# Optimization experiments

Hardware: AMD Instinct MI355X
Metric: run time of the kernel (lower is better)

## Reference

```python
import jax, jax.numpy as jnp
import numpy as np
from jax import lax

B_, H_, W_ = 2, 32, 32
D_MODEL, D_STATE, D_CONV, DT_RANK, K = 192, 16, 3, 12, 4
D_INNER = 2 * D_MODEL


def setup_inputs() -> dict:
    key = jax.random.key(0)
    ks = jax.random.split(key, 10)
    x = jax.random.normal(ks[0], (B_, H_, W_, D_MODEL), jnp.float32)
    x_cross = jax.random.normal(ks[1], (B_, H_, W_, D_MODEL), jnp.float32)
    in_proj_w = jax.random.normal(ks[2], (2 * D_INNER, D_MODEL), jnp.float32) * 0.02
    in_proj_cross_w = jax.random.normal(ks[3], (D_INNER, D_MODEL), jnp.float32) * 0.02
    conv_w = jax.random.normal(ks[4], (D_INNER, 1, D_CONV, D_CONV), jnp.float32) * 0.1  # depthwise
    conv_b = jnp.zeros((D_INNER,), jnp.float32)
    x_proj_weight = jax.random.normal(ks[5], (K, DT_RANK + 2 * D_STATE, D_INNER), jnp.float32) * 0.02
    dt_std = DT_RANK ** -0.5
    dt_projs_weight = jax.random.uniform(ks[6], (K, D_INNER, DT_RANK), jnp.float32, -dt_std, dt_std)
    # inverse-softplus init of dt bias, as in CSS2D.dt_init
    dt = jnp.exp(jax.random.uniform(ks[7], (K, D_INNER), jnp.float32)
                 * (np.log(0.1) - np.log(0.001)) + np.log(0.001))
    dt = jnp.clip(dt, 1e-4, None)
    dt_projs_bias = dt + jnp.log(-jnp.expm1(-dt))
    A_logs = jnp.log(jnp.tile(jnp.arange(1, D_STATE + 1, dtype=jnp.float32)[None, :], (K * D_INNER, 1)))
    Ds = jnp.ones((K * D_INNER,), jnp.float32)
    out_norm_g = jnp.ones((D_INNER,), jnp.float32)
    out_norm_b = jnp.zeros((D_INNER,), jnp.float32)
    out_proj_w = jax.random.normal(ks[8], (D_MODEL, D_INNER), jnp.float32) * 0.02
    return dict(x=x, x_cross=x_cross, in_proj_w=in_proj_w, in_proj_cross_w=in_proj_cross_w,
                conv_w=conv_w, conv_b=conv_b, x_proj_weight=x_proj_weight,
                dt_projs_weight=dt_projs_weight, dt_projs_bias=dt_projs_bias,
                A_logs=A_logs, Ds=Ds, out_norm_g=out_norm_g, out_norm_b=out_norm_b,
                out_proj_w=out_proj_w)


def _css2d_forward(x, x_cross, in_proj_w, in_proj_cross_w, conv_w, conv_b,
                   x_proj_weight, dt_projs_weight, dt_projs_bias, A_logs, Ds,
                   out_norm_g, out_norm_b, out_proj_w):
    B, H, W, _ = x.shape
    L = H * W
    Din, N, R = D_INNER, D_STATE, DT_RANK

    # in projections
    xz = x @ in_proj_w.T                       # [B,H,W,2*Din]
    xp, z = jnp.split(xz, 2, axis=-1)
    xc = x_cross @ in_proj_cross_w.T           # [B,H,W,Din]

    # depthwise conv + SiLU on main branch (NCHW)
    xh = jnp.transpose(xp, (0, 3, 1, 2))
    pad = (D_CONV - 1) // 2
    xh = lax.conv_general_dilated(xh, conv_w, (1, 1), [(pad, pad), (pad, pad)],
                                  dimension_numbers=('NCHW', 'OIHW', 'NCHW'),
                                  feature_group_count=Din)
    xh = jax.nn.silu(xh + conv_b[None, :, None, None])
    xc = jnp.transpose(xc, (0, 3, 1, 2))       # [B,Din,H,W]

    def cross_scan(t):  # [B,Din,H,W] -> [B,4,Din,L]
        a = t.reshape(B, Din, L)
        b = jnp.transpose(t, (0, 1, 3, 2)).reshape(B, Din, L)
        s = jnp.stack([a, b], axis=1)
        return jnp.concatenate([s, jnp.flip(s, axis=-1)], axis=1)

    xs = cross_scan(xh)
    xsc = cross_scan(xc)

    # dt/B/C projections from the cross stream
    x_dbl = jnp.einsum('bkdl,kcd->bkcl', xsc, x_proj_weight)
    dts, Bmat, Cmat = jnp.split(x_dbl, [R, R + N], axis=2)  # [B,K,R,L],[B,K,N,L],[B,K,N,L]
    dts = jnp.einsum('bkrl,kdr->bkdl', dts, dt_projs_weight)

    A = -jnp.exp(A_logs).reshape(K, Din, N)
    delta = jax.nn.softplus(dts + dt_projs_bias[None, :, :, None])  # [B,K,Din,L]

    # selective scan: h_{t} = exp(delta*A)*h_{t-1} + delta*B_t*u_t ; y_t = C_t . h_t
    dA = jnp.exp(jnp.einsum('bkdl,kdn->lbkdn', delta, A))   # [L,B,K,Din,N]
    dBu = jnp.einsum('bkdl,bknl->lbkdn', delta * xs, Bmat)  # [L,B,K,Din,N]
    Ct = jnp.transpose(Cmat, (3, 0, 1, 2))                  # [L,B,K,N]

    def step(h, inp):
        dA_t, dBu_t, c = inp
        h = dA_t * h + dBu_t
        return h, jnp.einsum('bkdn,bkn->bkd', h, c)

    h0 = jnp.zeros((B, K, Din, N), x.dtype)
    _, ys = lax.scan(step, h0, (dA, dBu, Ct))               # ys: [L,B,K,Din]
    out_y = jnp.transpose(ys, (1, 2, 3, 0)) + xs * Ds.reshape(1, K, Din, 1)  # [B,K,Din,L]

    # merge the 4 directions
    inv_y = jnp.flip(out_y[:, 2:4], axis=-1)
    wh = lambda t: jnp.transpose(t.reshape(B, Din, W, H), (0, 1, 3, 2)).reshape(B, Din, L)
    y = out_y[:, 0] + inv_y[:, 0] + wh(out_y[:, 1]) + wh(inv_y[:, 1])
    y = jnp.transpose(y, (0, 2, 1)).reshape(B, H, W, Din)

    # LayerNorm(out_norm)
    mu = jnp.mean(y, axis=-1, keepdims=True)
    var = jnp.mean((y - mu) ** 2, axis=-1, keepdims=True)
    y = (y - mu) * lax.rsqrt(var + 1e-5) * out_norm_g + out_norm_b

    y = y * jax.nn.silu(z)
    return y @ out_proj_w.T


def reference(x, x_cross, in_proj_w, in_proj_cross_w, conv_w, conv_b, x_proj_weight,
              dt_projs_weight, dt_projs_bias, A_logs, Ds, out_norm_g, out_norm_b, out_proj_w):
    return _css2d_forward(x, x_cross, in_proj_w, in_proj_cross_w, conv_w, conv_b,
                          x_proj_weight, dt_projs_weight, dt_projs_bias, A_logs, Ds,
                          out_norm_g, out_norm_b, out_proj_w)
```

## Files before the change

### kernel.cpp

```cpp
#include <hip/hip_runtime.h>
#include <hip/hip_bf16.h>
#include <math.h>

#define BB 2
#define HH 32
#define WW 32
#define LL 1024
#define DM 192
#define DI 384
#define NS 16
#define RR 12
#define KK 4
#define CC 44
#define NC 64
#define LC 16
#define NCH 3072
#define GB 49152
#define XT 8

__device__ __forceinline__ int bfflag(const void* dsv){
  return ((const unsigned*)dsv)[0] != 0x3F800000u;
}
__device__ __forceinline__ float ldin(const void* p, int i, int bf) {
  if (bf) {
    unsigned v = ((const unsigned short*)p)[i];
    return __uint_as_float(v << 16);
  }
  return ((const float*)p)[i];
}
__device__ __forceinline__ float4 ldin4(const void* p, int i, int bf) {
  if (bf) {
    ushort4 u = ((const ushort4*)p)[i >> 2];
    float4 r;
    r.x = __uint_as_float((unsigned)u.x << 16);
    r.y = __uint_as_float((unsigned)u.y << 16);
    r.z = __uint_as_float((unsigned)u.z << 16);
    r.w = __uint_as_float((unsigned)u.w << 16);
    return r;
  }
  return ((const float4*)p)[i >> 2];
}
__device__ __forceinline__ float sigm(float x){ return 1.f/(1.f + __expf(-x)); }
__device__ __forceinline__ float softplusf(float x){ return (x > 20.f) ? x : log1pf(__expf(x)); }

__device__ __forceinline__ int permk(int k, int l){
  if (k == 0) return l;
  if (k == 2) return LL-1-l;
  int lr = (k == 3) ? (LL-1-l) : l;
  return (lr & 31)*WW + (lr >> 5);
}

__global__ __launch_bounds__(192) void k_inproj(const void* x, const void* xcr,
    const void* wi, const void* wc, const void* dsv,
    float* __restrict__ xp, float* __restrict__ z, float* __restrict__ xc){
  const int bf = bfflag(dsv);
  __shared__ float xs_[16][DM];
  const int t = threadIdx.x;
  const int rg = blockIdx.x / 128;
  const int pos0 = (blockIdx.x % 128) * 16;
  const void* src = (rg >= 4) ? xcr : x;
  for (int i = t*4; i < 16*DM; i += 192*4) {
    *(float4*)&(((float*)xs_)[i]) = ldin4(src, pos0*DM + i, bf);
  }
  __syncthreads();
  const int grow = rg*192 + t;
  const void* wb = (grow < 768) ? wi : wc;
  const int wrow = (grow < 768) ? grow : grow - 768;
  float* dst; int o;
  if (grow < 384)      { dst = xp; o = grow; }
  else if (grow < 768) { dst = z;  o = grow - 384; }
  else                 { dst = xc; o = grow - 768; }
  float acc[16];
  #pragma unroll
  for (int p=0;p<16;p++) acc[p]=0.f;
  for (int j=0;j<DM;j+=4) {
    const float4 w4 = ldin4(wb, wrow*DM + j, bf);
    #pragma unroll
    for (int p=0;p<16;p++){
      const float4 xv = *(const float4*)&xs_[p][j];
      acc[p] = fmaf(w4.x, xv.x, acc[p]);
      acc[p] = fmaf(w4.y, xv.y, acc[p]);
      acc[p] = fmaf(w4.z, xv.z, acc[p]);
      acc[p] = fmaf(w4.w, xv.w, acc[p]);
    }
  }
  #pragma unroll
  for (int p=0;p<16;p++) dst[(pos0+p)*DI + o] = acc[p];
}

__global__ __launch_bounds__(256) void k_conv(const float* __restrict__ xp,
    const void* cw, const void* cb, const void* dsv, float* __restrict__ xh){
  const int bf = bfflag(dsv);
  const int idx = blockIdx.x*256 + threadIdx.x;
  const int d = idx % DI;
  const int l = (idx / DI) % LL;
  const int b = idx / (DI*LL);
  const int h = l >> 5, w = l & 31;
  float acc = ldin(cb, d, bf);
  #pragma unroll
  for (int kh=0; kh<3; kh++){
    const int hh = h + kh - 1;
    if (hh < 0 || hh >= HH) continue;
    #pragma unroll
    for (int kw=0; kw<3; kw++){
      const int ww2 = w + kw - 1;
      if (ww2 < 0 || ww2 >= WW) continue;
      acc = fmaf(xp[(b*LL + hh*WW + ww2)*DI + d], ldin(cw, d*9 + kh*3 + kw, bf), acc);
    }
  }
  xh[idx] = acc * sigm(acc);
}

__global__ __launch_bounds__(384) void k_xproj(const float* __restrict__ xc, const void* xpw,
    const void* dtw, const void* dtb, const void* dsv,
    float* __restrict__ delta, float* __restrict__ Bm, float* __restrict__ Cm){
  const int bf = bfflag(dsv);
  const int blk = blockIdx.x;
  const int b = blk >> 9;
  const int k = (blk >> 7) & 3;
  const int l0 = (blk & 127) * XT;
  const int t = threadIdx.x;
  __shared__ float xrow[XT][DI+4];
  __shared__ float dtsS[XT][RR];
  for (int idx = t; idx < XT*96; idx += 384){
    const int j = idx / 96, c = idx % 96;
    const int pl = permk(k, l0 + j);
    *(float4*)&xrow[j][c*4] = *(const float4*)&xc[(b*LL + pl)*DI + c*4];
  }
  __syncthreads();
  if (t < CC*XT){
    const int ch = t >> 3, j = t & 7;
    const int wbase = (k*CC + ch)*DI;
    float a0=0.f, a1=0.f, a2=0.f, a3=0.f;
    for (int c = 0; c < 96; c += 4){
      const float4 w0 = ldin4(xpw, wbase + (c+0)*4, bf);
      const float4 w1 = ldin4(xpw, wbase + (c+1)*4, bf);
      const float4 w2 = ldin4(xpw, wbase + (c+2)*4, bf);
      const float4 w3 = ldin4(xpw, wbase + (c+3)*4, bf);
      const float4 x0 = *(const float4*)&xrow[j][(c+0)*4];
      const float4 x1 = *(const float4*)&xrow[j][(c+1)*4];
      const float4 x2 = *(const float4*)&xrow[j][(c+2)*4];
      const float4 x3 = *(const float4*)&xrow[j][(c+3)*4];
      a0 = fmaf(w0.x,x0.x, fmaf(w0.y,x0.y, fmaf(w0.z,x0.z, fmaf(w0.w,x0.w, a0))));
      a1 = fmaf(w1.x,x1.x, fmaf(w1.y,x1.y, fmaf(w1.z,x1.z, fmaf(w1.w,x1.w, a1))));
      a2 = fmaf(w2.x,x2.x, fmaf(w2.y,x2.y, fmaf(w2.z,x2.z, fmaf(w2.w,x2.w, a2))));
      a3 = fmaf(w3.x,x3.x, fmaf(w3.y,x3.y, fmaf(w3.z,x3.z, fmaf(w3.w,x3.w, a3))));
    }
    const float acc = (a0+a1)+(a2+a3);
    if (ch < RR)           dtsS[j][ch] = acc;
    else if (ch < RR+NS)   Bm[((b*KK+k)*LL + l0+j)*NS + (ch-RR)]    = acc;
    else                   Cm[((b*KK+k)*LL + l0+j)*NS + (ch-RR-NS)] = acc;
  }
  __syncthreads();
  {
    const int d = t;
    float w[RR];
    #pragma unroll
    for (int q = 0; q < 3; q++){
      const float4 w4 = ldin4(dtw, (k*DI+d)*RR + q*4, bf);
      w[q*4+0]=w4.x; w[q*4+1]=w4.y; w[q*4+2]=w4.z; w[q*4+3]=w4.w;
    }
    const float bias = ldin(dtb, k*DI + d, bf);
    #pragma unroll
    for (int j = 0; j < XT; j++){
      float acc = bias;
      #pragma unroll
      for (int r = 0; r < RR; r++) acc = fmaf(w[r], dtsS[j][r], acc);
      xrow[j][d] = softplusf(acc);
    }
  }
  __syncthreads();
  for (int idx = t; idx < XT*96; idx += 384){
    const int j = idx / 96, c = idx % 96;
    *(float4*)&delta[((b*KK+k)*LL + l0+j)*DI + c*4] = *(const float4*)&xrow[j][c*4];
  }
}

__global__ __launch_bounds__(256) void k_scanA(const float* __restrict__ delta,
    const float* __restrict__ xh, const float* __restrict__ Bm,
    const void* alogs, const void* dsv,
    float* __restrict__ Acum, float* __restrict__ Hend){
  const int bf = bfflag(dsv);
  const int c = blockIdx.x / 12;
  const int chain = (blockIdx.x % 12)*256 + threadIdx.x;
  const int d = chain % DI;
  const int k = (chain / DI) & 3;
  const int b = chain / (DI*KK);
  float An[NS];
  #pragma unroll
  for (int q = 0; q < 4; q++){
    const float4 a4 = ldin4(alogs, (k*DI + d)*NS + q*4, bf);
    An[q*4+0] = -__expf(a4.x); An[q*4+1] = -__expf(a4.y);
    An[q*4+2] = -__expf(a4.z); An[q*4+3] = -__expf(a4.w);
  }
  float h[NS], Ac[NS];
  #pragma unroll
  for (int n = 0; n < NS; n++){ h[n] = 0.f; Ac[n] = 1.f; }
  const int lb = (b*KK+k)*LL;
  const int xbase = b*LL*DI + d;
  const int l0 = c*LC;
  #pragma unroll 4
  for (int l = l0; l < l0+LC; l++){
    const float dl = delta[(lb + l)*DI + d];
    const float u  = xh[xbase + permk(k,l)*DI];
    const float dlu = dl*u;
    const float4 B0 = *(const float4*)&Bm[(lb+l)*NS + 0];
    const float4 B1 = *(const float4*)&Bm[(lb+l)*NS + 4];
    const float4 B2 = *(const float4*)&Bm[(lb+l)*NS + 8];
    const float4 B3 = *(const float4*)&Bm[(lb+l)*NS + 12];
    const float Bv[NS] = {B0.x,B0.y,B0.z,B0.w, B1.x,B1.y,B1.z,B1.w,
                          B2.x,B2.y,B2.z,B2.w, B3.x,B3.y,B3.z,B3.w};
    #pragma unroll
    for (int n = 0; n < NS; n++){
      const float e = __expf(dl*An[n]);
      Ac[n] *= e;
      h[n] = fmaf(e, h[n], dlu*Bv[n]);
    }
  }
  const int obase = (c*NCH + chain)*NS;
  #pragma unroll
  for (int q = 0; q < 4; q++){
    *(float4*)&Acum[obase + q*4] = make_float4(Ac[q*4],Ac[q*4+1],Ac[q*4+2],Ac[q*4+3]);
    *(float4*)&Hend[obase + q*4] = make_float4(h[q*4],h[q*4+1],h[q*4+2],h[q*4+3]);
  }
}

__global__ __launch_bounds__(256) void k_scanB(const float* __restrict__ Acum,
    float* __restrict__ Hend){
  const int g = blockIdx.x*256 + threadIdx.x;
  float h = 0.f;
  #pragma unroll 8
  for (int c = 0; c < NC; c++){
    const float a = Acum[c*GB + g];
    const float e = Hend[c*GB + g];
    Hend[c*GB + g] = h;
    h = fmaf(a, h, e);
  }
}

__global__ __launch_bounds__(256) void k_scanC(const float* __restrict__ delta,
    const float* __restrict__ xh, const float* __restrict__ Bm,
    const float* __restrict__ Cm, const void* alogs, const void* dsv,
    const float* __restrict__ Hin, float* __restrict__ ybuf){
  const int bf = bfflag(dsv);
  const int c = blockIdx.x / 12;
  const int chain = (blockIdx.x % 12)*256 + threadIdx.x;
  const int d = chain % DI;
  const int k = (chain / DI) & 3;
  const int b = chain / (DI*KK);
  float An[NS];
  #pragma unroll
  for (int q = 0; q < 4; q++){
    const float4 a4 = ldin4(alogs, (k*DI + d)*NS + q*4, bf);
    An[q*4+0] = -__expf(a4.x); An[q*4+1] = -__expf(a4.y);
    An[q*4+2] = -__expf(a4.z); An[q*4+3] = -__expf(a4.w);
  }
  float h[NS];
  const int ibase = (c*NCH + chain)*NS;
  #pragma unroll
  for (int q = 0; q < 4; q++){
    const float4 h4 = *(const float4*)&Hin[ibase + q*4];
    h[q*4+0]=h4.x; h[q*4+1]=h4.y; h[q*4+2]=h4.z; h[q*4+3]=h4.w;
  }
  const int lb = (b*KK+k)*LL;
  const int xbase = b*LL*DI + d;
  const int l0 = c*LC;
  #pragma unroll 4
  for (int l = l0; l < l0+LC; l++){
    const float dl = delta[(lb + l)*DI + d];
    const float u  = xh[xbase + permk(k,l)*DI];
    const float dlu = dl*u;
    const float4 B0 = *(const float4*)&Bm[(lb+l)*NS + 0];
    const float4 B1 = *(const float4*)&Bm[(lb+l)*NS + 4];
    const float4 B2 = *(const float4*)&Bm[(lb+l)*NS + 8];
    const float4 B3 = *(const float4*)&Bm[(lb+l)*NS + 12];
    const float4 C0 = *(const float4*)&Cm[(lb+l)*NS + 0];
    const float4 C1 = *(const float4*)&Cm[(lb+l)*NS + 4];
    const float4 C2 = *(const float4*)&Cm[(lb+l)*NS + 8];
    const float4 C3 = *(const float4*)&Cm[(lb+l)*NS + 12];
    const float Bv[NS] = {B0.x,B0.y,B0.z,B0.w, B1.x,B1.y,B1.z,B1.w,
                          B2.x,B2.y,B2.z,B2.w, B3.x,B3.y,B3.z,B3.w};
    const float Cv[NS] = {C0.x,C0.y,C0.z,C0.w, C1.x,C1.y,C1.z,C1.w,
                          C2.x,C2.y,C2.z,C2.w, C3.x,C3.y,C3.z,C3.w};
    float y = 0.f;
    #pragma unroll
    for (int n = 0; n < NS; n++){
      const float e = __expf(dl*An[n]);
      h[n] = fmaf(e, h[n], dlu*Bv[n]);
      y = fmaf(h[n], Cv[n], y);
    }
    ybuf[(lb + l)*DI + d] = y;
  }
}

__global__ __launch_bounds__(256) void k_merge(const float* __restrict__ scanY,
    const float* __restrict__ xh, const float* __restrict__ z,
    const void* dsP, const void* gP, const void* bP, const void* woP,
    void* out){
  const int bf = bfflag(dsP);
  const int blk = blockIdx.x;
  const int t = threadIdx.x;
  const int wv = t >> 6, lane = t & 63;
  __shared__ float ygs[8][DI];
  #pragma unroll
  for (int rep = 0; rep < 2; rep++){
    const int j = wv*2 + rep;
    const int pos = blk*8 + j;
    const int b = pos >> 10, l = pos & 1023;
    const int lt = (l & 31)*32 + (l >> 5);
    float yv[6];
    float s = 0.f, s2 = 0.f;
    #pragma unroll
    for (int i = 0; i < 6; i++){
      const int d = i*64 + lane;
      float y = scanY[((b*KK+0)*LL + l        )*DI + d]
              + scanY[((b*KK+2)*LL + (LL-1-l ))*DI + d]
              + scanY[((b*KK+1)*LL + lt       )*DI + d]
              + scanY[((b*KK+3)*LL + (LL-1-lt))*DI + d];
      const float dsum = ldin(dsP, d, bf) + ldin(dsP, DI+d, bf)
                       + ldin(dsP, 2*DI+d, bf) + ldin(dsP, 3*DI+d, bf);
      y = fmaf(xh[(b*LL+l)*DI + d], dsum, y);
      yv[i] = y;
      s += y; s2 = fmaf(y, y, s2);
    }
    #pragma unroll
    for (int m = 1; m < 64; m <<= 1){
      s  += __shfl_xor(s,  m);
      s2 += __shfl_xor(s2, m);
    }
    const float mu = s * (1.f/DI);
    const float var = fmaxf(s2 * (1.f/DI) - mu*mu, 0.f);
    const float rs = rsqrtf(var + 1e-5f);
    #pragma unroll
    for (int i = 0; i < 6; i++){
      const int d = i*64 + lane;
      const float yn = (yv[i]-mu)*rs*ldin(gP, d, bf) + ldin(bP, d, bf);
      const float zg = z[(b*LL+l)*DI + d];
      ygs[j][d] = yn * zg * sigm(zg);
    }
  }
  __syncthreads();
  if (t < DM){
    const int o = t;
    float acc[8];
    #pragma unroll
    for (int j=0;j<8;j++) acc[j] = 0.f;
    for (int c = 0; c < 96; c++){
      const float4 w4 = ldin4(woP, o*DI + c*4, bf);
      #pragma unroll
      for (int j=0;j<8;j++){
        const float4 y4 = *(const float4*)&ygs[j][c*4];
        acc[j] = fmaf(w4.x, y4.x, acc[j]);
        acc[j] = fmaf(w4.y, y4.y, acc[j]);
        acc[j] = fmaf(w4.z, y4.z, acc[j]);
        acc[j] = fmaf(w4.w, y4.w, acc[j]);
      }
    }
    #pragma unroll
    for (int j=0;j<8;j++){
      const int pos = blk*8 + j;
      if (bf) ((__hip_bfloat16*)out)[pos*DM + o] = __float2bfloat16(acc[j]);
      else    ((float*)out)[pos*DM + o] = acc[j];
    }
  }
}

extern "C" void kernel_launch(void* const* d_in, const int* in_sizes, int n_in,
                              void* d_out, int out_size, void* d_ws, size_t ws_size,
                              hipStream_t stream){
  const void* x    = d_in[0];
  const void* xcr  = d_in[1];
  const void* wi   = d_in[2];
  const void* wc   = d_in[3];
  const void* cw   = d_in[4];
  const void* cb   = d_in[5];
  const void* xpw  = d_in[6];
  const void* dtw  = d_in[7];
  const void* dtb  = d_in[8];
  const void* alog = d_in[9];
  const void* dsv  = d_in[10];
  const void* gno  = d_in[11];
  const void* bno  = d_in[12];
  const void* wo   = d_in[13];

  float* ws = (float*)d_ws;
  float* xp    = ws + 16;
  float* z     = xp    + (size_t)BB*LL*DI;
  float* xc    = z     + (size_t)BB*LL*DI;
  float* xh    = xc    + (size_t)BB*LL*DI;
  float* delta = xh    + (size_t)BB*LL*DI;
  float* Bm    = delta + (size_t)BB*KK*LL*DI;
  float* Cm    = Bm    + (size_t)BB*KK*LL*NS;
  float* Acum  = Cm    + (size_t)BB*KK*LL*NS;
  float* Hend  = Acum  + (size_t)GB*NC;
  float* ybuf  = Hend  + (size_t)GB*NC;

  k_inproj<<<6*128, 192, 0, stream>>>(x, xcr, wi, wc, dsv, xp, z, xc);
  k_conv  <<<BB*LL*DI/256, 256, 0, stream>>>(xp, cw, cb, dsv, xh);
  k_xproj <<<BB*KK*(LL/XT), 384, 0, stream>>>(xc, xpw, dtw, dtb, dsv, delta, Bm, Cm);
  k_scanA <<<NCH*NC/256, 256, 0, stream>>>(delta, xh, Bm, alog, dsv, Acum, Hend);
  k_scanB <<<GB/256, 256, 0, stream>>>(Acum, Hend);
  k_scanC <<<NCH*NC/256, 256, 0, stream>>>(delta, xh, Bm, Cm, alog, dsv, Hend, ybuf);
  k_merge <<<BB*LL/8, 256, 0, stream>>>(ybuf, xh, z, dsv, gno, bno, wo, d_out);
}
```

Baseline: 242.9 us.

## Tile in-projection GEMM with 64x64 shared-memory blocks and 4x4 register tiles

Rewrites the input projection kernel as a classic shared-memory tiled GEMM. Each block stages 64 positions and 64 weight rows per 64-wide K chunk and computes a 4x4 output tile per thread, writing results with float4 stores. Previously every thread streamed its own weight row from global memory with no reuse and wrote scattered scalars. The new version adds transposed shared-memory stores (padded to 65) that can cause bank conflicts, and the float4 reads from the padded rows may be misaligned.

```diff
diff --git a/kernel.cpp b/kernel.cpp
--- a/kernel.cpp
+++ b/kernel.cpp
@@ -50,42 +50,61 @@
   return (lr & 31)*WW + (lr >> 5);
 }
 
-__global__ __launch_bounds__(192) void k_inproj(const void* x, const void* xcr,
+__global__ __launch_bounds__(256) void k_inproj(const void* x, const void* xcr,
     const void* wi, const void* wc, const void* dsv,
-    float* __restrict__ xp, float* __restrict__ z, float* __restrict__ xc){
+    float* __restrict__ xp, float* __restrict__ z, float* __restrict__ xcd){
   const int bf = bfflag(dsv);
-  __shared__ float xs_[16][DM];
+  __shared__ float As[64][65];
+  __shared__ float Ws[64][65];
+  const int mb = blockIdx.x & 31;
+  const int nb = blockIdx.x >> 5;
+  const int pos0 = mb*64;
+  const int row0g = nb*64;
+  const void* src  = (row0g < 768) ? x  : xcr;
+  const void* wsrc = (row0g < 768) ? wi : wc;
+  const int wrow0 = (row0g < 768) ? row0g : row0g - 768;
   const int t = threadIdx.x;
-  const int rg = blockIdx.x / 128;
-  const int pos0 = (blockIdx.x % 128) * 16;
-  const void* src = (rg >= 4) ? xcr : x;
-  for (int i = t*4; i < 16*DM; i += 192*4) {
-    *(float4*)&(((float*)xs_)[i]) = ldin4(src, pos0*DM + i, bf);
-  }
-  __syncthreads();
-  const int grow = rg*192 + t;
-  const void* wb = (grow < 768) ? wi : wc;
-  const int wrow = (grow < 768) ? grow : grow - 768;
-  float* dst; int o;
-  if (grow < 384)      { dst = xp; o = grow; }
-  else if (grow < 768) { dst = z;  o = grow - 384; }
-  else                 { dst = xc; o = grow - 768; }
-  float acc[16];
-  #pragma unroll
-  for (int p=0;p<16;p++) acc[p]=0.f;
-  for (int j=0;j<DM;j+=4) {
-    const float4 w4 = ldin4(wb, wrow*DM + j, bf);
-    #pragma unroll
-    for (int p=0;p<16;p++){
-      const float4 xv = *(const float4*)&xs_[p][j];
-      acc[p] = fmaf(w4.x, xv.x, acc[p]);
-      acc[p] = fmaf(w4.y, xv.y, acc[p]);
-      acc[p] = fmaf(w4.z, xv.z, acc[p]);
-      acc[p] = fmaf(w4.w, xv.w, acc[p]);
-    }
-  }
-  #pragma unroll
-  for (int p=0;p<16;p++) dst[(pos0+p)*DI + o] = acc[p];
+  const int tx = t & 15, ty = t >> 4;
+  float acc[4][4];
+  #pragma unroll
+  for (int m=0;m<4;m++){
+    #pragma unroll
+    for (int n=0;n<4;n++) acc[m][n]=0.f;
+  }
+  for (int k0 = 0; k0 < DM; k0 += 64){
+    for (int i = t*4; i < 4096; i += 1024){
+      const int p = i >> 6, kk = i & 63;
+      const float4 va = ldin4(src,  (pos0 +p)*DM + k0 + kk, bf);
+      As[kk+0][p]=va.x; As[kk+1][p]=va.y; As[kk+2][p]=va.z; As[kk+3][p]=va.w;
+      const float4 vw = ldin4(wsrc, (wrow0+p)*DM + k0 + kk, bf);
+      Ws[kk+0][p]=vw.x; Ws[kk+1][p]=vw.y; Ws[kk+2][p]=vw.z; Ws[kk+3][p]=vw.w;
+    }
+    __syncthreads();
+    #pragma unroll 8
+    for (int kk = 0; kk < 64; kk++){
+      const float4 a4 = *(const float4*)&As[kk][ty*4];
+      const float4 w4 = *(const float4*)&Ws[kk][tx*4];
+      acc[0][0]=fmaf(a4.x,w4.x,acc[0][0]); acc[0][1]=fmaf(a4.x,w4.y,acc[0][1]);
+      acc[0][2]=fmaf(a4.x,w4.z,acc[0][2]); acc[0][3]=fmaf(a4.x,w4.w,acc[0][3]);
+      acc[1][0]=fmaf(a4.y,w4.x,acc[1][0]); acc[1][1]=fmaf(a4.y,w4.y,acc[1][1]);
+      acc[1][2]=fmaf(a4.y,w4.z,acc[1][2]); acc[1][3]=fmaf(a4.y,w4.w,acc[1][3]);
+      acc[2][0]=fmaf(a4.z,w4.x,acc[2][0]); acc[2][1]=fmaf(a4.z,w4.y,acc[2][1]);
+      acc[2][2]=fmaf(a4.z,w4.z,acc[2][2]); acc[2][3]=fmaf(a4.z,w4.w,acc[2][3]);
+      acc[3][0]=fmaf(a4.w,w4.x,acc[3][0]); acc[3][1]=fmaf(a4.w,w4.y,acc[3][1]);
+      acc[3][2]=fmaf(a4.w,w4.z,acc[3][2]); acc[3][3]=fmaf(a4.w,w4.w,acc[3][3]);
+    }
+    __syncthreads();
+  }
+  float* dst; int obase;
+  if (row0g < 384)      { dst = xp;  obase = row0g; }
+  else if (row0g < 768) { dst = z;   obase = row0g-384; }
+  else                  { dst = xcd; obase = row0g-768; }
+  #pragma unroll
+  for (int m=0;m<4;m++){
+    const int pos = pos0 + ty*4 + m;
+    *(float4*)&dst[(size_t)pos*DI + obase + tx*4] =
+        make_float4(acc[m][0], acc[m][1], acc[m][2], acc[m][3]);
+  }
 }
 
 __global__ __launch_bounds__(256) void k_conv(const float* __restrict__ xp,
@@ -395,7 +414,7 @@
   float* Hend  = Acum  + (size_t)GB*NC;
   float* ybuf  = Hend  + (size_t)GB*NC;
 
-  k_inproj<<<6*128, 192, 0, stream>>>(x, xcr, wi, wc, dsv, xp, z, xc);
+  k_inproj<<<18*32, 256, 0, stream>>>(x, xcr, wi, wc, dsv, xp, z, xc);
   k_conv  <<<BB*LL*DI/256, 256, 0, stream>>>(xp, cw, cb, dsv, xh);
   k_xproj <<<BB*KK*(LL/XT), 384, 0, stream>>>(xc, xpw, dtw, dtb, dsv, delta, Bm, Cm);
   k_scanA <<<NCH*NC/256, 256, 0, stream>>>(delta, xh, Bm, alog, dsv, Acum, Hend);
```

After: 231.6 us. -4.6%, faster.
